# Performance work log

Hardware: AMD Instinct MI355X
Metric: run time of the kernel (lower is better)

## Reference

```python
import jax, jax.numpy as jnp
import numpy as np

N = 262144
H = 128            # hidden_features
NB = 8             # hidden_layers
CD = 128           # c_dim // 2
ENC_P = 3 * 2 * 10 + 3   # 63
ENC_V = 3 * 2 * 4 + 3    # 27


def encode_points(p, L):
    # concat [p, sin(2^i p), cos(2^i p)] for i in 0..L-1, matching torch concat order
    freqs = 2.0 ** jnp.arange(L, dtype=p.dtype)            # [L]
    ang = p[..., None, :] * freqs[:, None]                 # [..., L, 3]
    sc = jnp.concatenate([jnp.sin(ang), jnp.cos(ang)], axis=-1)  # [..., L, 6]
    sc = sc.reshape(*p.shape[:-1], L * 2 * p.shape[-1])
    return jnp.concatenate([p, sc], axis=-1)


def setup_inputs() -> dict:
    key = jax.random.key(0)
    ks = jax.random.split(key, 24)
    s = 0.05
    inp = {
        "coords": (jax.random.uniform(ks[0], (N, 3)) * 2.0 - 1.0) * 3.0,  # in (-pi, pi)
        "condition": jax.random.normal(ks[1], (N, 2 * CD)),
        "ray_dir": jax.random.normal(ks[2], (N, 3)),
        "noise": jax.random.normal(ks[3], (N, 1)),
        "W_in": jax.random.normal(ks[4], (ENC_P, H)) * s, "b_in": jnp.zeros((H,)),
        "W_blocks": jax.random.normal(ks[5], (NB, H, H)) * s, "b_blocks": jnp.zeros((NB, H)),
        "W_c": jax.random.normal(ks[6], (CD, H)) * s, "b_c": jnp.zeros((H,)),
        "W_skip": jax.random.normal(ks[7], (ENC_P, H)) * s, "b_skip": jnp.zeros((H,)),
        "W_skipc": jax.random.normal(ks[8], (CD, H)) * s, "b_skipc": jnp.zeros((H,)),
        "W_out": jax.random.normal(ks[9], (H, 1)) * s, "b_out": jnp.zeros((1,)),
        "W_viewc": jax.random.normal(ks[10], (CD, H)) * s, "b_viewc": jnp.zeros((H,)),
        "W_view": jax.random.normal(ks[11], (ENC_V, H)) * s, "b_view": jnp.zeros((H,)),
        "W_rgb": jax.random.normal(ks[12], (H, 3)) * s, "b_rgb": jnp.zeros((3,)),
    }
    return inp


def reference(coords, condition, ray_dir, noise,
              W_in, b_in, W_blocks, b_blocks, W_c, b_c,
              W_skip, b_skip, W_skipc, b_skipc, W_out, b_out,
              W_viewc, b_viewc, W_view, b_view, W_rgb, b_rgb):
    relu = jax.nn.relu
    cond_shape, cond_app = condition[..., :CD], condition[..., CD:]
    enc = encode_points(coords, 10)                       # [N, 63]
    net = enc @ W_in + b_in + (cond_shape @ W_c + b_c)
    for idx in range(NB):
        if idx == 4:  # skips=[4]
            net = net + (enc @ W_skip + b_skip) + (cond_shape @ W_skipc + b_skipc)
        net = relu(net) @ W_blocks[idx] + b_blocks[idx]
    sigma = relu(net) @ W_out + b_out                     # density_offset = 0
    sigma = sigma + noise * 1.0                           # raw_noise_std = 1.0
    sigma = relu(sigma)                                   # activate_sigma
    rd = ray_dir / jnp.linalg.norm(ray_dir, axis=-1, keepdims=True)
    enc_v = encode_points(rd, 4)                          # [N, 27]
    net = net + (enc_v @ W_view + b_view) + (cond_app @ W_viewc + b_viewc)
    rgb = jax.nn.sigmoid(relu(net) @ W_rgb + b_rgb)       # net_view: ReLU -> Linear(128,3)
    return jnp.concatenate([sigma, rgb], axis=-1)
```

## Files before the change

### kernel.cpp

```cpp
#include <hip/hip_runtime.h>
#include <hip/hip_bf16.h>

typedef unsigned int u32;
typedef unsigned short u16;

using bf16x8 = __attribute__((ext_vector_type(8))) short;
using f32x4  = __attribute__((ext_vector_type(4))) float;

#define OFF_IN    0L
#define OFF_SKIP  18432L
#define OFF_VIEW  36864L
#define HOFF(i)   (47104L + (long)(i) * 32768L)

#define LDS_X   0
#define LDS_S0  34816
#define LDS_S1  53248
#define LDS_SP  69632
#define LDS_RP  70656
#define LDS_B   73728
#define LDS_TOTAL 79360
#define BB(i)   (1536 + (i) * 512)

__device__ __forceinline__ u16 f2bf(float x) {
  union { float f; u32 u; } un; un.f = x;
  u32 u = un.u;
  return (u16)((u + 0x7fffu + ((u >> 16) & 1u)) >> 16);
}
__device__ __forceinline__ u32 pack2(float a, float b) {
  u32 r;
  asm("v_cvt_pk_bf16_f32 %0, %1, %2" : "=v"(r) : "v"(a), "v"(b));
  return r;
}
__device__ __forceinline__ float sel3(float a, float b, float c, int i) {
  return i == 0 ? a : (i == 1 ? b : c);
}
__device__ __forceinline__ float enc_val3(float a, float b, float c, int e, int kreal) {
  if (e >= kreal) return 0.f;
  if (e < 3) return sel3(a, b, c, e);
  int t = e - 3;
  int l = t / 6;
  int rem = t - l * 6;
  int pi = rem >= 3 ? rem - 3 : rem;
  float x = sel3(a, b, c, pi) * (float)(1 << l);
  return rem < 3 ? __sinf(x) : __cosf(x);
}
__device__ __forceinline__ bf16x8 mk8(u32 a, u32 b, u32 c, u32 d) {
  union { u32 u[4]; bf16x8 v; } t; t.u[0] = a; t.u[1] = b; t.u[2] = c; t.u[3] = d;
  return t.v;
}
__device__ __forceinline__ void gll16(const void* g, void* l) {
  __builtin_amdgcn_global_load_lds(
      (const __attribute__((address_space(1))) void*)g,
      (__attribute__((address_space(3))) void*)l, 16, 0, 0);
}
#define MFMA __builtin_amdgcn_mfma_f32_16x16x32_bf16
#define SBAR __builtin_amdgcn_s_barrier
#define SCHED0() __builtin_amdgcn_sched_barrier(0)
#define PRIO(n) __builtin_amdgcn_s_setprio(n)

__global__ void prep_kernel(
    const float* __restrict__ Win, const float* __restrict__ Wc, const float* __restrict__ Wb,
    const float* __restrict__ Wskip, const float* __restrict__ Wskipc,
    const float* __restrict__ Wview, const float* __restrict__ Wviewc,
    char* __restrict__ ws) {
  int i = blockIdx.x * 256 + threadIdx.x;
  if (i >= 203776) return;
  int r = i;
  const float* src;
  if (r < 9216)                  { src = Win;
    int n = r / 72, c = r % 72;
    float v = (c < 63) ? src[(long)c * 128 + n] : 0.f;
    *(u16*)(ws + OFF_IN + ((long)n * 72 + c) * 2) = f2bf(v); return; }
  else if ((r -= 9216) < 9216)   { src = Wskip;
    int n = r / 72, c = r % 72;
    float v = (c < 63) ? src[(long)c * 128 + n] : 0.f;
    *(u16*)(ws + OFF_SKIP + ((long)n * 72 + c) * 2) = f2bf(v); return; }
  else if ((r -= 9216) < 5120)   { src = Wview;
    int n = r / 40, c = r % 40;
    float v = (c < 27) ? src[(long)c * 128 + n] : 0.f;
    *(u16*)(ws + OFF_VIEW + ((long)n * 40 + c) * 2) = f2bf(v); return; }
  r -= 5120;
  int hi = r / 16384; r %= 16384;
  src = hi == 0 ? Wc : hi <= 4 ? Wb + (long)(hi - 1) * 16384
      : hi == 5 ? Wskipc : hi <= 9 ? Wb + (long)(hi - 2) * 16384 : Wviewc;
  long hbase = HOFF(hi);
  int c = r >> 13;
  int rr = r & 8191;
  int n = rr / 64, k0 = rr % 64;
  float v = src[(long)(64 * c + k0) * 128 + n];
  long boff = (long)n * 128 + ((k0 * 2) ^ ((n & 7) << 4));
  *(u16*)(ws + hbase + (long)c * 16384 + boff) = f2bf(v);
}

#define GLL_H(woff, lbase)                                                     \
  do {                                                                         \
    gll16(ws + (woff) + wvu * 1024 + lane * 16, lds + (lbase) + wvu * 1024);   \
    gll16(ws + (woff) + 8192 + wvu * 1024 + lane * 16,                         \
          lds + (lbase) + 8192 + wvu * 1024);                                  \
  } while (0)

#define GLL_U(woff, lbase, nbytes)                                             \
  do {                                                                         \
    _Pragma("unroll") for (int it_ = 0; it_ < 3; ++it_) {                      \
      int o_ = it_ * 8192 + wvu * 1024;                                        \
      if (o_ < (nbytes))                                                       \
        gll16(ws + (woff) + o_ + lane * 16, lds + (lbase) + o_);               \
    }                                                                          \
  } while (0)

#define STREAM_COND(halfsel)                                                   \
  do {                                                                         \
    _Pragma("unroll") for (int c_ = 0; c_ < 2; ++c_) {                         \
      f32x4 v_[4];                                                             \
      _Pragma("unroll") for (int i2 = 0; i2 < 4; ++i2) {                       \
        int f4i = (4 * c_ + i2) * 512 + tid;                                   \
        int row = f4i >> 5, c4 = f4i & 31;                                     \
        v_[i2] = *(const f32x4*)(condition + (size_t)(p0 + row) * 256 +        \
                                 ((halfsel) * 32 + c4) * 4);                   \
      }                                                                        \
      _Pragma("unroll") for (int i2 = 0; i2 < 4; ++i2) {                       \
        int f4i = (4 * c_ + i2) * 512 + tid;                                   \
        int row = f4i >> 5, c4 = f4i & 31;                                     \
        uint2 t_; t_.x = pack2(v_[i2][0], v_[i2][1]);                          \
        t_.y = pack2(v_[i2][2], v_[i2][3]);                                    \
        *(uint2*)(lds + LDS_X + row * 272 + c4 * 8) = t_;                      \
      }                                                                        \
    }                                                                          \
  } while (0)

#define ENC_LOAD_COMPUTE(EF, LAUNDER)                                          \
  do {                                                                         \
    _Pragma("unroll") for (int mi_ = 0; mi_ < 2; ++mi_) {                      \
      int idx_ = p0 + 32 * wr + 16 * mi_ + li;                                 \
      if (LAUNDER) asm volatile("" : "+v"(idx_));                              \
      const float* cp_ = coords + (size_t)idx_ * 3;                            \
      float c0_ = cp_[0], c1_ = cp_[1], c2_ = cp_[2];                          \
      _Pragma("unroll") for (int kt_ = 0; kt_ < 2; ++kt_) {                    \
        u32 w_[4];                                                             \
        _Pragma("unroll") for (int e2_ = 0; e2_ < 4; ++e2_) {                  \
          int k0_ = kt_ * 32 + h * 8 + e2_ * 2;                                \
          w_[e2_] = pack2(enc_val3(c0_, c1_, c2_, k0_, 63),                    \
                          enc_val3(c0_, c1_, c2_, k0_ + 1, 63));               \
        }                                                                      \
        EF[mi_][kt_] = mk8(w_[0], w_[1], w_[2], w_[3]);                        \
      }                                                                        \
    }                                                                          \
  } while (0)

#define ACC_SET_LDS(BOFF)                                                      \
  do {                                                                         \
    _Pragma("unroll") for (int j = 0; j < 4; ++j) {                            \
      f32x4 b4_ = *(const f32x4*)(lds + LDS_B + (BOFF) + (64*wc + 16*j + 4*h) * 4); \
      _Pragma("unroll") for (int mi = 0; mi < 2; ++mi) acc[mi][j] = b4_;       \
    }                                                                          \
  } while (0)

#define ACC_ADD_LDS(BOFF)                                                      \
  do {                                                                         \
    _Pragma("unroll") for (int j = 0; j < 4; ++j) {                            \
      f32x4 b4_ = *(const f32x4*)(lds + LDS_B + (BOFF) + (64*wc + 16*j + 4*h) * 4); \
      _Pragma("unroll") for (int mi = 0; mi < 2; ++mi) acc[mi][j] += b4_;      \
    }                                                                          \
  } while (0)

#define GEMM_SWZ(SBASE, XO)                                                    \
  do {                                                                         \
    int swz_ = (li & 7) << 4;                                                  \
    PRIO(1);                                                                   \
    _Pragma("unroll") for (int kb = 0; kb < 2; ++kb) {                         \
      bf16x8 xf[2];                                                            \
      _Pragma("unroll") for (int mi = 0; mi < 2; ++mi)                         \
        xf[mi] = *(const bf16x8*)(lds + LDS_X + (32*wr + 16*mi + li) * 272 +   \
                                  (XO) + kb * 64 + h16);                       \
      _Pragma("unroll") for (int j = 0; j < 4; ++j) {                          \
        bf16x8 wf = *(const bf16x8*)(lds + (SBASE) + (64*wc + 16*j + li) * 128 \
                                     + ((kb * 64 + h16) ^ swz_));              \
        _Pragma("unroll") for (int mi = 0; mi < 2; ++mi)                       \
          acc[mi][j] = MFMA(wf, xf[mi], acc[mi][j], 0, 0, 0);                  \
      }                                                                        \
    }                                                                          \
    PRIO(0);                                                                   \
  } while (0)

#define GEMME01(EF)                                                            \
  do {                                                                         \
    PRIO(1);                                                                   \
    _Pragma("unroll") for (int j = 0; j < 4; ++j) {                            \
      const char* wrp = lds + LDS_S0 + (64*wc + 16*j + li) * 144 + h16;        \
      bf16x8 wf0 = *(const bf16x8*)(wrp);                                      \
      bf16x8 wf1 = *(const bf16x8*)(wrp + 64);                                 \
      _Pragma("unroll") for (int mi = 0; mi < 2; ++mi) {                       \
        acc[mi][j] = MFMA(wf0, EF[mi][0], acc[mi][j], 0, 0, 0);                \
        acc[mi][j] = MFMA(wf1, EF[mi][1], acc[mi][j], 0, 0, 0);                \
      }                                                                        \
    }                                                                          \
    PRIO(0);                                                                   \
  } while (0)

#define STORE_X()                                                              \
  do {                                                                         \
    _Pragma("unroll") for (int mi = 0; mi < 2; ++mi)                           \
    _Pragma("unroll") for (int j = 0; j < 4; ++j) {                            \
      f32x4 v_ = acc[mi][j];                                                   \
      uint2 t_;                                                                \
      t_.x = pack2(fmaxf(v_[0], 0.f), fmaxf(v_[1], 0.f));                      \
      t_.y = pack2(fmaxf(v_[2], 0.f), fmaxf(v_[3], 0.f));                      \
      *(uint2*)(lds + LDS_X + (32*wr + 16*mi + li) * 272 + (64*wc + 16*j + 4*h) * 2) = t_; \
    }                                                                          \
  } while (0)

#define PHASE_MID(BOFF, NOFF)                                                  \
  do {                                                                         \
    if ((BOFF) >= 0) ACC_SET_LDS(BOFF);                                        \
    GEMM_SWZ(LDS_S0, 0);                                                       \
    SBAR();                                                                    \
    GLL_H((NOFF), LDS_S0);                                                     \
    asm volatile("s_waitcnt vmcnt(2)" ::: "memory");        \
    SCHED0(); SBAR();                                                          \
    GEMM_SWZ(LDS_S1, 128);                                                     \
    SBAR();                                                                    \
    GLL_H((NOFF) + 16384, LDS_S1);                                             \
    asm volatile("s_waitcnt vmcnt(2)" ::: "memory");       \
    SCHED0();                                                                  \
    STORE_X();                                                                 \
    asm volatile("s_waitcnt lgkmcnt(0)" ::: "memory");                         \
    SCHED0(); SBAR();                                                          \
  } while (0)

#define PHASE_LAST(BOFF)                                                       \
  do {                                                                         \
    if ((BOFF) >= 0) ACC_SET_LDS(BOFF);                                        \
    GEMM_SWZ(LDS_S0, 0);                                                       \
    asm volatile("s_waitcnt vmcnt(0)" ::: "memory");                           \
    SCHED0(); SBAR();                                                          \
    GEMM_SWZ(LDS_S1, 128);                                                     \
  } while (0)

#define PRELOAD(NOFF)                                                          \
  do {                                                                         \
    GLL_H((NOFF), LDS_S0);                                                     \
    GLL_H((NOFF) + 16384, LDS_S1);                                             \
    asm volatile("s_waitcnt vmcnt(2)" ::: "memory");             \
    SCHED0(); SBAR();                                                          \
  } while (0)

__global__ void __launch_bounds__(512, 4) nerf_main(
    const float* __restrict__ coords, const float* __restrict__ condition,
    const float* __restrict__ ray_dir, const float* __restrict__ noise,
    const float* __restrict__ b_in, const float* __restrict__ b_c,
    const float* __restrict__ b_blocks, const float* __restrict__ b_skip,
    const float* __restrict__ b_skipc, const float* __restrict__ b_view,
    const float* __restrict__ b_viewc, const float* __restrict__ W_out,
    const float* __restrict__ b_out, const float* __restrict__ W_rgb,
    const float* __restrict__ b_rgb, const char* __restrict__ ws,
    float* __restrict__ out) {
  extern __shared__ __align__(16) char lds[];
  const int tid = threadIdx.x;
  const int lane = tid & 63;
  const int wvu = __builtin_amdgcn_readfirstlane(tid >> 6);
  const int wr = wvu >> 1, wc = wvu & 1;
  const int li = lane & 15, h = lane >> 4;
  const int h16 = h * 16;
  const int p0 = blockIdx.x * 128;

  f32x4 acc[2][4];

#pragma unroll
  for (int it = 0; it < 3; ++it) {
    int i = tid + it * 512;
    if (i < 1408) {
      float v = i < 128 ? b_in[i] + b_c[i]
              : i < 256 ? b_skip[i - 128] + b_skipc[i - 128]
              : i < 384 ? b_view[i - 256] + b_viewc[i - 256]
              : b_blocks[i - 384];
      *(float*)(lds + LDS_B + (long)i * 4) = v;
    }
  }
  STREAM_COND(0);
  GLL_U(OFF_IN, LDS_S0, 18432);
  __syncthreads();

  {
    bf16x8 encf[2][2];
    ENC_LOAD_COMPUTE(encf, 0);
    ACC_SET_LDS(0);
    GEMME01(encf);
  }
  __syncthreads();

  PRELOAD(HOFF(0));
  PHASE_MID(-1, HOFF(1));
  PHASE_MID(BB(0), HOFF(2));
  PHASE_MID(BB(1), HOFF(3));
  PHASE_MID(BB(2), HOFF(4));
  PHASE_LAST(BB(3));

  GLL_U(OFF_SKIP, LDS_S0, 18432);
  __syncthreads();
  STREAM_COND(0);
  __syncthreads();

  {
    bf16x8 encf[2][2];
    ENC_LOAD_COMPUTE(encf, 1);
    ACC_ADD_LDS(512);
    GEMME01(encf);
  }
  __syncthreads();

  PRELOAD(HOFF(5));
  PHASE_MID(-1, HOFF(6));
  PHASE_MID(BB(4), HOFF(7));
  PHASE_MID(BB(5), HOFF(8));
  PHASE_MID(BB(6), HOFF(9));
  PHASE_LAST(BB(7));

#pragma unroll
  for (int mi = 0; mi < 2; ++mi) {
    float s = 0.f;
#pragma unroll
    for (int j = 0; j < 4; ++j) {
      f32x4 wo = *(const f32x4*)(W_out + 64 * wc + 16 * j + 4 * h);
#pragma unroll
      for (int rr = 0; rr < 4; ++rr) s += fmaxf(acc[mi][j][rr], 0.f) * wo[rr];
    }
    s += __shfl_xor(s, 16); s += __shfl_xor(s, 32);
    if (h == 0) *(float*)(lds + LDS_SP + ((32 * wr + 16 * mi + li) * 2 + wc) * 4) = s;
  }
  __syncthreads();
  GLL_U(OFF_VIEW, LDS_S0, 10240);
  STREAM_COND(1);
  __syncthreads();
  if (tid < 128) {
    const float* sp = (const float*)(lds + LDS_SP);
    float s = sp[2 * tid] + sp[2 * tid + 1] + b_out[0] + noise[p0 + tid];
    out[(size_t)(p0 + tid) * 4] = fmaxf(s, 0.f);
  }

  {
    bf16x8 envf[2];
#pragma unroll
    for (int mi = 0; mi < 2; ++mi) {
      size_t base = (size_t)(p0 + 32 * wr + 16 * mi + li) * 3;
      float r0 = ray_dir[base], r1 = ray_dir[base + 1], r2 = ray_dir[base + 2];
      float inv = 1.f / sqrtf(r0 * r0 + r1 * r1 + r2 * r2);
      r0 *= inv; r1 *= inv; r2 *= inv;
      u32 w[4];
#pragma unroll
      for (int e2 = 0; e2 < 4; ++e2) {
        int k0 = h * 8 + e2 * 2;
        w[e2] = pack2(enc_val3(r0, r1, r2, k0, 27), enc_val3(r0, r1, r2, k0 + 1, 27));
      }
      envf[mi] = mk8(w[0], w[1], w[2], w[3]);
    }
    ACC_ADD_LDS(1024);
    PRIO(1);
#pragma unroll
    for (int j = 0; j < 4; ++j) {
      bf16x8 wf = *(const bf16x8*)(lds + LDS_S0 + (64 * wc + 16 * j + li) * 80 + h16);
#pragma unroll
      for (int mi = 0; mi < 2; ++mi)
        acc[mi][j] = MFMA(wf, envf[mi], acc[mi][j], 0, 0, 0);
    }
    PRIO(0);
  }
  __syncthreads();

  PRELOAD(HOFF(10));
  PHASE_LAST(-1);

#pragma unroll
  for (int mi = 0; mi < 2; ++mi) {
    float s0 = 0.f, s1 = 0.f, s2 = 0.f;
#pragma unroll
    for (int j = 0; j < 4; ++j)
#pragma unroll
      for (int rr = 0; rr < 4; ++rr) {
        float v = fmaxf(acc[mi][j][rr], 0.f);
        int n = 64 * wc + 16 * j + 4 * h + rr;
        s0 += v * W_rgb[n * 3 + 0];
        s1 += v * W_rgb[n * 3 + 1];
        s2 += v * W_rgb[n * 3 + 2];
      }
    s0 += __shfl_xor(s0, 16); s0 += __shfl_xor(s0, 32);
    s1 += __shfl_xor(s1, 16); s1 += __shfl_xor(s1, 32);
    s2 += __shfl_xor(s2, 16); s2 += __shfl_xor(s2, 32);
    if (h == 0) {
      float* rp = (float*)(lds + LDS_RP);
      int m_ = 32 * wr + 16 * mi + li;
      rp[(m_ * 2 + wc) * 3 + 0] = s0;
      rp[(m_ * 2 + wc) * 3 + 1] = s1;
      rp[(m_ * 2 + wc) * 3 + 2] = s2;
    }
  }
  __syncthreads();
  if (tid < 128) {
    const float* rp = (const float*)(lds + LDS_RP);
#pragma unroll
    for (int c = 0; c < 3; ++c) {
      float v = rp[(2 * tid) * 3 + c] + rp[(2 * tid + 1) * 3 + c] + b_rgb[c];
      out[(size_t)(p0 + tid) * 4 + 1 + c] = 1.f / (1.f + __expf(-v));
    }
  }
}

extern "C" void kernel_launch(void* const* d_in, const int* in_sizes, int n_in,
                              void* d_out, int out_size, void* d_ws, size_t ws_size,
                              hipStream_t stream) {
  const float* coords    = (const float*)d_in[0];
  const float* condition = (const float*)d_in[1];
  const float* ray_dir   = (const float*)d_in[2];
  const float* noise     = (const float*)d_in[3];
  const float* W_in      = (const float*)d_in[4];
  const float* b_in      = (const float*)d_in[5];
  const float* W_blocks  = (const float*)d_in[6];
  const float* b_blocks  = (const float*)d_in[7];
  const float* W_c       = (const float*)d_in[8];
  const float* b_c       = (const float*)d_in[9];
  const float* W_skip    = (const float*)d_in[10];
  const float* b_skip    = (const float*)d_in[11];
  const float* W_skipc   = (const float*)d_in[12];
  const float* b_skipc   = (const float*)d_in[13];
  const float* W_out     = (const float*)d_in[14];
  const float* b_out     = (const float*)d_in[15];
  const float* W_viewc   = (const float*)d_in[16];
  const float* b_viewc   = (const float*)d_in[17];
  const float* W_view    = (const float*)d_in[18];
  const float* b_view    = (const float*)d_in[19];
  const float* W_rgb     = (const float*)d_in[20];
  const float* b_rgb     = (const float*)d_in[21];
  char* ws = (char*)d_ws;
  float* out = (float*)d_out;

  prep_kernel<<<796, 256, 0, stream>>>(W_in, W_c, W_blocks, W_skip, W_skipc,
                                       W_view, W_viewc, ws);
  nerf_main<<<2048, 512, LDS_TOTAL, stream>>>(coords, condition, ray_dir, noise,
                                              b_in, b_c, b_blocks, b_skip, b_skipc,
                                              b_view, b_viewc, W_out, b_out,
                                              W_rgb, b_rgb, ws, out);
}
```

Before: 174.5 us.

## Shrink blocks to 64 points with single-buffered weights and global biases

Halves the block size to 256 threads and 64 points per block, doubling the grid. The LDS footprint is cut to roughly half by using one 16KB weight staging buffer instead of two. Biases are pre-summed in the prep kernel and read from global memory instead of being staged in LDS. The double-buffered vmcnt-based pipelining is replaced with plain __syncthreads, trading load/compute overlap for higher occupancy and simpler sync, but weights are now reloaded twice as often per point.

Result: slower. 188.6 us (+8.1%).

```diff
diff --git a/kernel.cpp b/kernel.cpp
--- a/kernel.cpp
+++ b/kernel.cpp
@@ -11,15 +11,15 @@
 #define OFF_SKIP  18432L
 #define OFF_VIEW  36864L
 #define HOFF(i)   (47104L + (long)(i) * 32768L)
+#define OFF_B0S   407552L
+#define OFF_BSK   408064L
+#define OFF_BV    408576L
 
 #define LDS_X   0
-#define LDS_S0  34816
-#define LDS_S1  53248
-#define LDS_SP  69632
-#define LDS_RP  70656
-#define LDS_B   73728
-#define LDS_TOTAL 79360
-#define BB(i)   (1536 + (i) * 512)
+#define LDS_W   17408
+#define LDS_SP  35840
+#define LDS_RP  36352
+#define LDS_TOTAL 37888
 
 __device__ __forceinline__ u16 f2bf(float x) {
   union { float f; u32 u; } un; un.f = x;
@@ -54,17 +54,18 @@
       (__attribute__((address_space(3))) void*)l, 16, 0, 0);
 }
 #define MFMA __builtin_amdgcn_mfma_f32_16x16x32_bf16
-#define SBAR __builtin_amdgcn_s_barrier
-#define SCHED0() __builtin_amdgcn_sched_barrier(0)
 #define PRIO(n) __builtin_amdgcn_s_setprio(n)
 
 __global__ void prep_kernel(
     const float* __restrict__ Win, const float* __restrict__ Wc, const float* __restrict__ Wb,
     const float* __restrict__ Wskip, const float* __restrict__ Wskipc,
     const float* __restrict__ Wview, const float* __restrict__ Wviewc,
+    const float* __restrict__ bin, const float* __restrict__ bc,
+    const float* __restrict__ bskip, const float* __restrict__ bskipc,
+    const float* __restrict__ bview, const float* __restrict__ bviewc,
     char* __restrict__ ws) {
   int i = blockIdx.x * 256 + threadIdx.x;
-  if (i >= 203776) return;
+  if (i >= 204160) return;
   int r = i;
   const float* src;
   if (r < 9216)                  { src = Win;
@@ -79,32 +80,40 @@
     int n = r / 40, c = r % 40;
     float v = (c < 27) ? src[(long)c * 128 + n] : 0.f;
     *(u16*)(ws + OFF_VIEW + ((long)n * 40 + c) * 2) = f2bf(v); return; }
-  r -= 5120;
-  int hi = r / 16384; r %= 16384;
-  src = hi == 0 ? Wc : hi <= 4 ? Wb + (long)(hi - 1) * 16384
-      : hi == 5 ? Wskipc : hi <= 9 ? Wb + (long)(hi - 2) * 16384 : Wviewc;
-  long hbase = HOFF(hi);
-  int c = r >> 13;
-  int rr = r & 8191;
-  int n = rr / 64, k0 = rr % 64;
-  float v = src[(long)(64 * c + k0) * 128 + n];
-  long boff = (long)n * 128 + ((k0 * 2) ^ ((n & 7) << 4));
-  *(u16*)(ws + hbase + (long)c * 16384 + boff) = f2bf(v);
-}
-
-#define GLL_H(woff, lbase)                                                     \
-  do {                                                                         \
-    gll16(ws + (woff) + wvu * 1024 + lane * 16, lds + (lbase) + wvu * 1024);   \
-    gll16(ws + (woff) + 8192 + wvu * 1024 + lane * 16,                         \
-          lds + (lbase) + 8192 + wvu * 1024);                                  \
-  } while (0)
-
-#define GLL_U(woff, lbase, nbytes)                                             \
-  do {                                                                         \
-    _Pragma("unroll") for (int it_ = 0; it_ < 3; ++it_) {                      \
-      int o_ = it_ * 8192 + wvu * 1024;                                        \
+  else if ((r -= 5120) < 180224) {
+    int hi = r / 16384; r %= 16384;
+    src = hi == 0 ? Wc : hi <= 4 ? Wb + (long)(hi - 1) * 16384
+        : hi == 5 ? Wskipc : hi <= 9 ? Wb + (long)(hi - 2) * 16384 : Wviewc;
+    long hbase = HOFF(hi);
+    int c = r >> 13;
+    int rr = r & 8191;
+    int n = rr / 64, k0 = rr % 64;
+    float v = src[(long)(64 * c + k0) * 128 + n];
+    long boff = (long)n * 128 + ((k0 * 2) ^ ((n & 7) << 4));
+    *(u16*)(ws + hbase + (long)c * 16384 + boff) = f2bf(v);
+    return;
+  }
+  r -= 180224;
+  int which = r >> 7, n = r & 127;
+  const float* A  = which == 0 ? bin : (which == 1 ? bskip : bview);
+  const float* Bp = which == 0 ? bc  : (which == 1 ? bskipc : bviewc);
+  long off = which == 0 ? OFF_B0S : (which == 1 ? OFF_BSK : OFF_BV);
+  *(float*)(ws + off + (long)n * 4) = A[n] + Bp[n];
+}
+
+#define GLL16K(woff)                                                           \
+  do {                                                                         \
+    _Pragma("unroll") for (int it_ = 0; it_ < 4; ++it_)                        \
+      gll16(ws + (woff) + it_ * 4096 + wvu * 1024 + lane * 16,                 \
+            lds + LDS_W + it_ * 4096 + wvu * 1024);                            \
+  } while (0)
+
+#define GLL_U(woff, nbytes)                                                    \
+  do {                                                                         \
+    _Pragma("unroll") for (int it_ = 0; it_ < 5; ++it_) {                      \
+      int o_ = it_ * 4096 + wvu * 1024;                                        \
       if (o_ < (nbytes))                                                       \
-        gll16(ws + (woff) + o_ + lane * 16, lds + (lbase) + o_);               \
+        gll16(ws + (woff) + o_ + lane * 16, lds + LDS_W + o_);                 \
     }                                                                          \
   } while (0)
 
@@ -113,13 +122,13 @@
     _Pragma("unroll") for (int c_ = 0; c_ < 2; ++c_) {                         \
       f32x4 v_[4];                                                             \
       _Pragma("unroll") for (int i2 = 0; i2 < 4; ++i2) {                       \
-        int f4i = (4 * c_ + i2) * 512 + tid;                                   \
+        int f4i = (4 * c_ + i2) * 256 + tid;                                   \
         int row = f4i >> 5, c4 = f4i & 31;                                     \
         v_[i2] = *(const f32x4*)(condition + (size_t)(p0 + row) * 256 +        \
                                  ((halfsel) * 32 + c4) * 4);                   \
       }                                                                        \
       _Pragma("unroll") for (int i2 = 0; i2 < 4; ++i2) {                       \
-        int f4i = (4 * c_ + i2) * 512 + tid;                                   \
+        int f4i = (4 * c_ + i2) * 256 + tid;                                   \
         int row = f4i >> 5, c4 = f4i & 31;                                     \
         uint2 t_; t_.x = pack2(v_[i2][0], v_[i2][1]);                          \
         t_.y = pack2(v_[i2][2], v_[i2][3]);                                    \
@@ -147,23 +156,23 @@
     }                                                                          \
   } while (0)
 
-#define ACC_SET_LDS(BOFF)                                                      \
+#define ACC_SET_G(bptr)                                                        \
   do {                                                                         \
     _Pragma("unroll") for (int j = 0; j < 4; ++j) {                            \
-      f32x4 b4_ = *(const f32x4*)(lds + LDS_B + (BOFF) + (64*wc + 16*j + 4*h) * 4); \
+      f32x4 b4_ = *(const f32x4*)((bptr) + 64*wc + 16*j + 4*h);                \
       _Pragma("unroll") for (int mi = 0; mi < 2; ++mi) acc[mi][j] = b4_;       \
     }                                                                          \
   } while (0)
 
-#define ACC_ADD_LDS(BOFF)                                                      \
+#define ACC_ADD_G(bptr)                                                        \
   do {                                                                         \
     _Pragma("unroll") for (int j = 0; j < 4; ++j) {                            \
-      f32x4 b4_ = *(const f32x4*)(lds + LDS_B + (BOFF) + (64*wc + 16*j + 4*h) * 4); \
+      f32x4 b4_ = *(const f32x4*)((bptr) + 64*wc + 16*j + 4*h);                \
       _Pragma("unroll") for (int mi = 0; mi < 2; ++mi) acc[mi][j] += b4_;      \
     }                                                                          \
   } while (0)
 
-#define GEMM_SWZ(SBASE, XO)                                                    \
+#define GEMM_SWZ(XO)                                                           \
   do {                                                                         \
     int swz_ = (li & 7) << 4;                                                  \
     PRIO(1);                                                                   \
@@ -173,7 +182,7 @@
         xf[mi] = *(const bf16x8*)(lds + LDS_X + (32*wr + 16*mi + li) * 272 +   \
                                   (XO) + kb * 64 + h16);                       \
       _Pragma("unroll") for (int j = 0; j < 4; ++j) {                          \
-        bf16x8 wf = *(const bf16x8*)(lds + (SBASE) + (64*wc + 16*j + li) * 128 \
+        bf16x8 wf = *(const bf16x8*)(lds + LDS_W + (64*wc + 16*j + li) * 128   \
                                      + ((kb * 64 + h16) ^ swz_));              \
         _Pragma("unroll") for (int mi = 0; mi < 2; ++mi)                       \
           acc[mi][j] = MFMA(wf, xf[mi], acc[mi][j], 0, 0, 0);                  \
@@ -182,11 +191,11 @@
     PRIO(0);                                                                   \
   } while (0)
 
-#define GEMME01(EF)                                                            \
+#define GEMME01(EF, WSTR)                                                      \
   do {                                                                         \
     PRIO(1);                                                                   \
     _Pragma("unroll") for (int j = 0; j < 4; ++j) {                            \
-      const char* wrp = lds + LDS_S0 + (64*wc + 16*j + li) * 144 + h16;        \
+      const char* wrp = lds + LDS_W + (64*wc + 16*j + li) * (WSTR) + h16;      \
       bf16x8 wf0 = *(const bf16x8*)(wrp);                                      \
       bf16x8 wf1 = *(const bf16x8*)(wrp + 64);                                 \
       _Pragma("unroll") for (int mi = 0; mi < 2; ++mi) {                       \
@@ -209,48 +218,24 @@
     }                                                                          \
   } while (0)
 
-#define PHASE_MID(BOFF, NOFF)                                                  \
-  do {                                                                         \
-    if ((BOFF) >= 0) ACC_SET_LDS(BOFF);                                        \
-    GEMM_SWZ(LDS_S0, 0);                                                       \
-    SBAR();                                                                    \
-    GLL_H((NOFF), LDS_S0);                                                     \
-    asm volatile("s_waitcnt vmcnt(2)" ::: "memory");        \
-    SCHED0(); SBAR();                                                          \
-    GEMM_SWZ(LDS_S1, 128);                                                     \
-    SBAR();                                                                    \
-    GLL_H((NOFF) + 16384, LDS_S1);                                             \
-    asm volatile("s_waitcnt vmcnt(2)" ::: "memory");       \
-    SCHED0();                                                                  \
-    STORE_X();                                                                 \
-    asm volatile("s_waitcnt lgkmcnt(0)" ::: "memory");                         \
-    SCHED0(); SBAR();                                                          \
-  } while (0)
-
-#define PHASE_LAST(BOFF)                                                       \
-  do {                                                                         \
-    if ((BOFF) >= 0) ACC_SET_LDS(BOFF);                                        \
-    GEMM_SWZ(LDS_S0, 0);                                                       \
-    asm volatile("s_waitcnt vmcnt(0)" ::: "memory");                           \
-    SCHED0(); SBAR();                                                          \
-    GEMM_SWZ(LDS_S1, 128);                                                     \
-  } while (0)
-
-#define PRELOAD(NOFF)                                                          \
-  do {                                                                         \
-    GLL_H((NOFF), LDS_S0);                                                     \
-    GLL_H((NOFF) + 16384, LDS_S1);                                             \
-    asm volatile("s_waitcnt vmcnt(2)" ::: "memory");             \
-    SCHED0(); SBAR();                                                          \
-  } while (0)
-
-__global__ void __launch_bounds__(512, 4) nerf_main(
+#define PHASE_HEAVY(BPTR, HI, NOFF, DOSTORE)                                   \
+  do {                                                                         \
+    if ((const void*)(BPTR) != nullptr) ACC_SET_G((const float*)(BPTR));       \
+    GEMM_SWZ(0);                                                               \
+    __syncthreads();                                                           \
+    GLL16K(HOFF(HI) + 16384);                                                  \
+    __syncthreads();                                                           \
+    GEMM_SWZ(128);                                                             \
+    __syncthreads();                                                           \
+    if (DOSTORE) STORE_X();                                                    \
+    if ((NOFF) >= 0) GLL16K(HOFF(NOFF));                                       \
+    __syncthreads();                                                           \
+  } while (0)
+
+__global__ void __launch_bounds__(256, 4) nerf_main(
     const float* __restrict__ coords, const float* __restrict__ condition,
     const float* __restrict__ ray_dir, const float* __restrict__ noise,
-    const float* __restrict__ b_in, const float* __restrict__ b_c,
-    const float* __restrict__ b_blocks, const float* __restrict__ b_skip,
-    const float* __restrict__ b_skipc, const float* __restrict__ b_view,
-    const float* __restrict__ b_viewc, const float* __restrict__ W_out,
+    const float* __restrict__ b_blocks, const float* __restrict__ W_out,
     const float* __restrict__ b_out, const float* __restrict__ W_rgb,
     const float* __restrict__ b_rgb, const char* __restrict__ ws,
     float* __restrict__ out) {
@@ -261,59 +246,49 @@
   const int wr = wvu >> 1, wc = wvu & 1;
   const int li = lane & 15, h = lane >> 4;
   const int h16 = h * 16;
-  const int p0 = blockIdx.x * 128;
+  const int p0 = blockIdx.x * 64;
 
   f32x4 acc[2][4];
 
-#pragma unroll
-  for (int it = 0; it < 3; ++it) {
-    int i = tid + it * 512;
-    if (i < 1408) {
-      float v = i < 128 ? b_in[i] + b_c[i]
-              : i < 256 ? b_skip[i - 128] + b_skipc[i - 128]
-              : i < 384 ? b_view[i - 256] + b_viewc[i - 256]
-              : b_blocks[i - 384];
-      *(float*)(lds + LDS_B + (long)i * 4) = v;
-    }
-  }
   STREAM_COND(0);
-  GLL_U(OFF_IN, LDS_S0, 18432);
+  GLL_U(OFF_IN, 18432);
   __syncthreads();
 
   {
     bf16x8 encf[2][2];
     ENC_LOAD_COMPUTE(encf, 0);
-    ACC_SET_LDS(0);
-    GEMME01(encf);
-  }
-  __syncthreads();
-
-  PRELOAD(HOFF(0));
-  PHASE_MID(-1, HOFF(1));
-  PHASE_MID(BB(0), HOFF(2));
-  PHASE_MID(BB(1), HOFF(3));
-  PHASE_MID(BB(2), HOFF(4));
-  PHASE_LAST(BB(3));
-
-  GLL_U(OFF_SKIP, LDS_S0, 18432);
-  __syncthreads();
+    ACC_SET_G((const float*)(ws + OFF_B0S));
+    GEMME01(encf, 144);
+  }
+  __syncthreads();
+  GLL16K(HOFF(0));
+  __syncthreads();
+
+  PHASE_HEAVY(nullptr, 0, 1, 1);
+  PHASE_HEAVY(b_blocks + 0 * 128, 1, 2, 1);
+  PHASE_HEAVY(b_blocks + 1 * 128, 2, 3, 1);
+  PHASE_HEAVY(b_blocks + 2 * 128, 3, 4, 1);
+  PHASE_HEAVY(b_blocks + 3 * 128, 4, -1, 0);
+
+  GLL_U(OFF_SKIP, 18432);
   STREAM_COND(0);
   __syncthreads();
 
   {
     bf16x8 encf[2][2];
     ENC_LOAD_COMPUTE(encf, 1);
-    ACC_ADD_LDS(512);
-    GEMME01(encf);
-  }
-  __syncthreads();
-
-  PRELOAD(HOFF(5));
-  PHASE_MID(-1, HOFF(6));
-  PHASE_MID(BB(4), HOFF(7));
-  PHASE_MID(BB(5), HOFF(8));
-  PHASE_MID(BB(6), HOFF(9));
-  PHASE_LAST(BB(7));
+    ACC_ADD_G((const float*)(ws + OFF_BSK));
+    GEMME01(encf, 144);
+  }
+  __syncthreads();
+  GLL16K(HOFF(5));
+  __syncthreads();
+
+  PHASE_HEAVY(nullptr, 5, 6, 1);
+  PHASE_HEAVY(b_blocks + 4 * 128, 6, 7, 1);
+  PHASE_HEAVY(b_blocks + 5 * 128, 7, 8, 1);
+  PHASE_HEAVY(b_blocks + 6 * 128, 8, 9, 1);
+  PHASE_HEAVY(b_blocks + 7 * 128, 9, -1, 0);
 
 #pragma unroll
   for (int mi = 0; mi < 2; ++mi) {
@@ -327,11 +302,10 @@
     s += __shfl_xor(s, 16); s += __shfl_xor(s, 32);
     if (h == 0) *(float*)(lds + LDS_SP + ((32 * wr + 16 * mi + li) * 2 + wc) * 4) = s;
   }
-  __syncthreads();
-  GLL_U(OFF_VIEW, LDS_S0, 10240);
+  GLL_U(OFF_VIEW, 10240);
   STREAM_COND(1);
   __syncthreads();
-  if (tid < 128) {
+  if (tid < 64) {
     const float* sp = (const float*)(lds + LDS_SP);
     float s = sp[2 * tid] + sp[2 * tid + 1] + b_out[0] + noise[p0 + tid];
     out[(size_t)(p0 + tid) * 4] = fmaxf(s, 0.f);
@@ -353,11 +327,11 @@
       }
       envf[mi] = mk8(w[0], w[1], w[2], w[3]);
     }
-    ACC_ADD_LDS(1024);
+    ACC_ADD_G((const float*)(ws + OFF_BV));
     PRIO(1);
 #pragma unroll
     for (int j = 0; j < 4; ++j) {
-      bf16x8 wf = *(const bf16x8*)(lds + LDS_S0 + (64 * wc + 16 * j + li) * 80 + h16);
+      bf16x8 wf = *(const bf16x8*)(lds + LDS_W + (64 * wc + 16 * j + li) * 80 + h16);
 #pragma unroll
       for (int mi = 0; mi < 2; ++mi)
         acc[mi][j] = MFMA(wf, envf[mi], acc[mi][j], 0, 0, 0);
@@ -365,9 +339,10 @@
     PRIO(0);
   }
   __syncthreads();
-
-  PRELOAD(HOFF(10));
-  PHASE_LAST(-1);
+  GLL16K(HOFF(10));
+  __syncthreads();
+
+  PHASE_HEAVY(nullptr, 10, -1, 0);
 
 #pragma unroll
   for (int mi = 0; mi < 2; ++mi) {
@@ -394,7 +369,7 @@
     }
   }
   __syncthreads();
-  if (tid < 128) {
+  if (tid < 64) {
     const float* rp = (const float*)(lds + LDS_RP);
 #pragma unroll
     for (int c = 0; c < 3; ++c) {
@@ -432,10 +407,10 @@
   char* ws = (char*)d_ws;
   float* out = (float*)d_out;
 
-  prep_kernel<<<796, 256, 0, stream>>>(W_in, W_c, W_blocks, W_skip, W_skipc,
-                                       W_view, W_viewc, ws);
-  nerf_main<<<2048, 512, LDS_TOTAL, stream>>>(coords, condition, ray_dir, noise,
-                                              b_in, b_c, b_blocks, b_skip, b_skipc,
-                                              b_view, b_viewc, W_out, b_out,
+  prep_kernel<<<798, 256, 0, stream>>>(W_in, W_c, W_blocks, W_skip, W_skipc,
+                                       W_view, W_viewc, b_in, b_c, b_skip,
+                                       b_skipc, b_view, b_viewc, ws);
+  nerf_main<<<4096, 256, LDS_TOTAL, stream>>>(coords, condition, ray_dir, noise,
+                                              b_blocks, W_out, b_out,
                                               W_rgb, b_rgb, ws, out);
 }
```
